# Kernel tuning notes

Measured on AMD Instinct MI355X. Metric: run time of the kernel, lower is better.

## Reference

```python
import jax, jax.numpy as jnp
import numpy as np

D_MODEL = 1024
N_HEADS = 16
D_KEYS = 64
D_LLM = 4096
B, L, S = 8, 1024, 1000
HD = N_HEADS * D_KEYS  # 1024


def setup_inputs() -> dict:
    key = jax.random.key(0)
    ks = jax.random.split(key, 12)
    sd = lambda fan_in: 1.0 / np.sqrt(fan_in)
    return {
        "target_embedding": jax.random.normal(ks[0], (B, L, D_MODEL), jnp.float32),
        "source_embedding": jax.random.normal(ks[1], (S, D_LLM), jnp.float32),
        "value_embedding": jax.random.normal(ks[2], (S, D_LLM), jnp.float32),
        "Wq": jax.random.normal(ks[3], (D_MODEL, HD), jnp.float32) * sd(D_MODEL),
        "bq": jnp.zeros((HD,), jnp.float32),
        "Wk": jax.random.normal(ks[4], (D_LLM, HD), jnp.float32) * sd(D_LLM),
        "bk": jnp.zeros((HD,), jnp.float32),
        "Wv": jax.random.normal(ks[5], (D_LLM, HD), jnp.float32) * sd(D_LLM),
        "bv": jnp.zeros((HD,), jnp.float32),
        "Wo": jax.random.normal(ks[6], (HD, D_LLM), jnp.float32) * sd(HD),
        "bo": jnp.zeros((D_LLM,), jnp.float32),
        "alpha": jnp.asarray(1.0, jnp.float32),
        "beta": jnp.asarray(0.5, jnp.float32),
    }


def reference(target_embedding, source_embedding, value_embedding,
              Wq, bq, Wk, bk, Wv, bv, Wo, bo, alpha, beta):
    # Projections
    q = (target_embedding @ Wq + bq).reshape(B, L, N_HEADS, D_KEYS)   # blhe
    k = (source_embedding @ Wk + bk).reshape(S, N_HEADS, D_KEYS)      # she
    v = (value_embedding @ Wv + bv).reshape(S, N_HEADS, D_KEYS)       # she
    # Reprogramming attention with alpha/beta scaling
    scale = 1.0 / np.sqrt(D_KEYS)
    scores = jnp.einsum('blhe,she->bhls', alpha * q, beta * k)        # BxHxLxS
    A = jax.nn.softmax(scale * scores, axis=-1)  # dropout is identity in eval
    out = jnp.einsum('bhls,she->blhe', A, v)
    out = out.reshape(B, L, HD)
    return out @ Wo + bo                                              # B,L,d_llm
```

## Files before the change

kernel.cpp:

```cpp
#include <hip/hip_runtime.h>

typedef unsigned short u16;
typedef __attribute__((ext_vector_type(8))) short short8;
typedef __attribute__((ext_vector_type(4))) float floatx4;

#define LOG2E 1.4426950408889634f

__device__ __forceinline__ u16 f2bf(float f) {
    unsigned u = __builtin_bit_cast(unsigned, f);
    u += 0x7fffu + ((u >> 16) & 1u);
    return (u16)(u >> 16);
}

__device__ __forceinline__ void gl2lds16(const void* g, void* l) {
    __builtin_amdgcn_global_load_lds((const __attribute__((address_space(1))) void*)g,
                                     (__attribute__((address_space(3))) void*)l,
                                     16, 0, 0);
}

__global__ __launch_bounds__(256) void conv_all(const float* __restrict__ T, u16* __restrict__ Tb,
                                                const float* __restrict__ Se, u16* __restrict__ Seb,
                                                const float* __restrict__ Ve, u16* __restrict__ Veb) {
    int g = blockIdx.x * 256 + threadIdx.x;
    const float* s; u16* d; int i; int nsrc;
    if (g < 2097152)      { s = T;  d = Tb;  i = g * 4;               nsrc = 8388608; }
    else if (g < 3145728) { s = Se; d = Seb; i = (g - 2097152) * 4;   nsrc = 4096000; }
    else                  { s = Ve; d = Veb; i = (g - 3145728) * 4;   nsrc = 4096000; }
    ushort4 o;
    if (i < nsrc) {
        float4 v = *(const float4*)(s + i);
        o.x = f2bf(v.x); o.y = f2bf(v.y); o.z = f2bf(v.z); o.w = f2bf(v.w);
    } else {
        o = make_ushort4(0, 0, 0, 0);
    }
    *(ushort4*)(d + i) = o;
}

__device__ __forceinline__ void transpose_core(const float* __restrict__ W, u16* __restrict__ Wt,
                                               int Kd, int Nd, int kx, int ny) {
    __shared__ u16 t[64][65];
    const int tid = threadIdx.x;
    const int k0 = kx * 64, n0 = ny * 64;
#pragma unroll
    for (int i = 0; i < 16; i++) {
        int r = i * 4 + (tid >> 6), c = tid & 63;
        t[r][c] = f2bf(W[(size_t)(k0 + r) * Nd + n0 + c]);
    }
    __syncthreads();
#pragma unroll
    for (int i = 0; i < 16; i++) {
        int n = i * 4 + (tid >> 6), k = tid & 63;
        Wt[(size_t)(n0 + n) * Kd + k0 + k] = t[k][n];
    }
}

__global__ __launch_bounds__(256) void transpose3(const float* __restrict__ Wq, u16* __restrict__ WqT,
                                                  const float* __restrict__ Wk, u16* __restrict__ WkT,
                                                  const float* __restrict__ Wv, u16* __restrict__ WvT) {
    int id = blockIdx.x;
    if (id < 256)       transpose_core(Wq, WqT, 1024, 1024, id & 15, id >> 4);
    else if (id < 1280) { int t = id - 256;  transpose_core(Wk, WkT, 4096, 1024, t & 63, t >> 6); }
    else                { int t = id - 1280; transpose_core(Wv, WvT, 4096, 1024, t & 63, t >> 6); }
}


__device__ __forceinline__ short8 ldsfrag(const u16* b, int row, int kk, int quad, int l7) {
    return *(const short8*)&b[row * 64 + (((kk * 4 + quad) ^ l7) * 8)];
}

__device__ __forceinline__
void stage_tile(u16* dA, u16* dB, const u16* gA, const u16* gB, int Ks, int wave, int lane) {
    int rl = wave * 8 + (lane >> 3);
    int cs = ((lane & 7) ^ (rl & 7)) * 8;
#pragma unroll
    for (int ii = 0; ii < 4; ii++) {
        gl2lds16(gA + (size_t)(ii * 64 + rl) * Ks + cs, dA + ii * 4096 + wave * 512);
        gl2lds16(gB + (size_t)(ii * 64 + rl) * Ks + cs, dB + ii * 4096 + wave * 512);
    }
}

__device__ __forceinline__
void four_phases(const u16* sA, const u16* sB, floatx4 (&acc)[8][4],
                 int wm, int wn, int quad, int l16, int l7,
                 bool stage, u16* dA, u16* dB, const u16* gA, const u16* gB, int Ks,
                 int wave, int lane) {
    short8 af[4][2], b0[2][2], b1[2][2];
    const int ra = wm * 128 + l16, rb = wn * 64 + l16;

#pragma unroll
    for (int i = 0; i < 4; i++) {
        af[i][0] = ldsfrag(sA, ra + i * 16, 0, quad, l7);
        af[i][1] = ldsfrag(sA, ra + i * 16, 1, quad, l7);
    }
#pragma unroll
    for (int j = 0; j < 2; j++) {
        b0[j][0] = ldsfrag(sB, rb + j * 16, 0, quad, l7);
        b0[j][1] = ldsfrag(sB, rb + j * 16, 1, quad, l7);
    }
    if (stage) stage_tile(dA, dB, gA, gB, Ks, wave, lane);
    __builtin_amdgcn_s_barrier();
    __builtin_amdgcn_s_setprio(1);
#pragma unroll
    for (int k = 0; k < 2; k++)
#pragma unroll
        for (int i = 0; i < 4; i++)
#pragma unroll
            for (int j = 0; j < 2; j++)
                acc[i][j] = __builtin_amdgcn_mfma_f32_16x16x32_bf16(af[i][k], b0[j][k], acc[i][j], 0, 0, 0);
    __builtin_amdgcn_s_setprio(0);
    __builtin_amdgcn_s_barrier();

#pragma unroll
    for (int j = 0; j < 2; j++) {
        b1[j][0] = ldsfrag(sB, rb + (j + 2) * 16, 0, quad, l7);
        b1[j][1] = ldsfrag(sB, rb + (j + 2) * 16, 1, quad, l7);
    }
    __builtin_amdgcn_s_barrier();
    __builtin_amdgcn_s_setprio(1);
#pragma unroll
    for (int k = 0; k < 2; k++)
#pragma unroll
        for (int i = 0; i < 4; i++)
#pragma unroll
            for (int j = 0; j < 2; j++)
                acc[i][j + 2] = __builtin_amdgcn_mfma_f32_16x16x32_bf16(af[i][k], b1[j][k], acc[i][j + 2], 0, 0, 0);
    __builtin_amdgcn_s_setprio(0);
    __builtin_amdgcn_s_barrier();

#pragma unroll
    for (int i = 0; i < 4; i++) {
        af[i][0] = ldsfrag(sA, ra + (i + 4) * 16, 0, quad, l7);
        af[i][1] = ldsfrag(sA, ra + (i + 4) * 16, 1, quad, l7);
    }
    __builtin_amdgcn_s_barrier();
    __builtin_amdgcn_s_setprio(1);
#pragma unroll
    for (int k = 0; k < 2; k++)
#pragma unroll
        for (int i = 0; i < 4; i++)
#pragma unroll
            for (int j = 0; j < 2; j++)
                acc[i + 4][j + 2] = __builtin_amdgcn_mfma_f32_16x16x32_bf16(af[i][k], b1[j][k], acc[i + 4][j + 2], 0, 0, 0);
    __builtin_amdgcn_s_setprio(0);
    __builtin_amdgcn_s_barrier();

    __builtin_amdgcn_s_setprio(1);
#pragma unroll
    for (int k = 0; k < 2; k++)
#pragma unroll
        for (int i = 0; i < 4; i++)
#pragma unroll
            for (int j = 0; j < 2; j++)
                acc[i + 4][j] = __builtin_amdgcn_mfma_f32_16x16x32_bf16(af[i][k], b0[j][k], acc[i + 4][j], 0, 0, 0);
    __builtin_amdgcn_s_setprio(0);
}

__device__ __forceinline__
void gemm8_core(const u16* __restrict__ A, const u16* __restrict__ Bt,
                const float* __restrict__ bias, void* __restrict__ Cout,
                int M, int N, int Ks, int Klen, int koff,
                int mode, float mult, int m0, int n0, u16* lds) {
    const int tid = threadIdx.x;
    const int wave = tid >> 6, lane = tid & 63;
    const int quad = lane >> 4, l16 = lane & 15, l7 = l16 & 7;
    const int wm = wave >> 2, wn = wave & 3;

    u16* A0 = lds;          u16* B0 = lds + 16384;
    u16* A1 = lds + 32768;  u16* B1 = lds + 49152;

    floatx4 acc[8][4];
#pragma unroll
    for (int i = 0; i < 8; i++)
#pragma unroll
        for (int j = 0; j < 4; j++) acc[i][j] = (floatx4){0.f, 0.f, 0.f, 0.f};

    const u16* Ag = A + (size_t)m0 * Ks + koff;
    const u16* Bg = Bt + (size_t)n0 * Ks + koff;

    stage_tile(A0, B0, Ag, Bg, Ks, wave, lane);
    asm volatile("s_waitcnt vmcnt(0)" ::: "memory");
    __builtin_amdgcn_sched_barrier(0);
    __builtin_amdgcn_s_barrier();

    const int NIT = Klen >> 7;
#pragma unroll 1
    for (int it = 0; it < NIT; ++it) {
        four_phases(A0, B0, acc, wm, wn, quad, l16, l7,
                    true, A1, B1, Ag + (2 * it + 1) * 64, Bg + (2 * it + 1) * 64, Ks, wave, lane);
        asm volatile("s_waitcnt vmcnt(0)" ::: "memory");
        __builtin_amdgcn_sched_barrier(0);
        __builtin_amdgcn_s_barrier();
        four_phases(A1, B1, acc, wm, wn, quad, l16, l7,
                    it + 1 < NIT, A0, B0, Ag + (2 * it + 2) * 64, Bg + (2 * it + 2) * 64, Ks, wave, lane);
        asm volatile("s_waitcnt vmcnt(0)" ::: "memory");
        __builtin_amdgcn_sched_barrier(0);
        __builtin_amdgcn_s_barrier();
    }

#pragma unroll
    for (int i = 0; i < 8; i++) {
#pragma unroll
        for (int j = 0; j < 4; j++) {
            int col = n0 + wn * 64 + j * 16 + l16;
            float bvv = (mode >= 4) ? 0.0f : bias[col];
#pragma unroll
            for (int r = 0; r < 4; r++) {
                int row = m0 + wm * 128 + i * 16 + quad * 4 + r;
                float v = (acc[i][j][r] + bvv) * mult;
                if (mode == 3 || mode == 4) {
                    ((float*)Cout)[(size_t)row * N + col] = v;
                } else if (mode == 5) {
                    ((float*)Cout)[(size_t)col * M + row] = v;
                } else {
                    ((u16*)Cout)[(size_t)row * N + col] = f2bf(v);
                }
            }
        }
    }
}

__global__ __launch_bounds__(512, 2)
void gemm_qkv(const u16* __restrict__ Tb, const u16* __restrict__ WqT, const float* __restrict__ bq,
              const u16* __restrict__ Seb, const u16* __restrict__ WkT,
              const u16* __restrict__ Veb, const u16* __restrict__ WvT,
              u16* __restrict__ Qb, float* __restrict__ KP, float* __restrict__ VPT,
              const float* __restrict__ alphaP, const float* __restrict__ betaP) {
    __shared__ u16 lds[65536];
    int b0 = blockIdx.x;
    int w = (b0 & 7) * 32 + (b0 >> 3);
    if (w < 128) {
        float mult = alphaP[0] * betaP[0] * 0.125f * LOG2E;
        gemm8_core(Tb, WqT, bq, Qb, 8192, 1024, 1024, 1024, 0,
                   1, mult, (w >> 2) * 256, (w & 3) * 256, lds);
    } else if (w < 192) {
        int t = w - 128; int kc = t >> 4;
        gemm8_core(Seb, WkT, nullptr, KP + (size_t)kc * 1048576, 1024, 1024, 4096, 1024, kc * 1024,
                   4, 1.0f, ((t >> 2) & 3) * 256, (t & 3) * 256, lds);
    } else {
        int t = w - 192; int kc = t >> 4;
        gemm8_core(Veb, WvT, nullptr, VPT + (size_t)kc * 1048576, 1024, 1024, 4096, 1024, kc * 1024,
                   5, 1.0f, ((t >> 2) & 3) * 256, (t & 3) * 256, lds);
    }
}

__global__ __launch_bounds__(512, 2)
void gemm_final(const u16* __restrict__ A, const u16* __restrict__ Bt,
                const float* __restrict__ bias, float* __restrict__ Cout) {
    __shared__ u16 lds[65536];
    int b0 = blockIdx.x;
    int idx = b0 >> 3;
    int m = (b0 & 7) * 4 + (idx >> 4);
    int n = idx & 15;
    gemm8_core(A, Bt, bias, Cout, 8192, 4096, 1024, 1024, 0, 3, 1.0f, m * 256, n * 256, lds);
}

__global__ __launch_bounds__(256)
void reduce_wo(const float* __restrict__ KP, const float* __restrict__ bk, u16* __restrict__ Kb,
               const float* __restrict__ VPT, const float* __restrict__ bv, u16* __restrict__ VTb,
               const float* __restrict__ Wo, u16* __restrict__ WoT) {
    int id = blockIdx.x;
    if (id >= 2048) {
        int t = id - 2048;
        transpose_core(Wo, WoT, 1024, 4096, t & 15, t >> 4);
        return;
    }
    const int tid = threadIdx.x;
    if (id < 1024) {
        int r = id, c = tid * 4;
        size_t base = (size_t)r * 1024 + c;
        float4 a0 = *(const float4*)(KP + base);
        float4 a1 = *(const float4*)(KP + 1048576 + base);
        float4 a2 = *(const float4*)(KP + 2097152 + base);
        float4 a3 = *(const float4*)(KP + 3145728 + base);
        float4 bb = *(const float4*)(bk + c);
        ushort4 o;
        o.x = f2bf(a0.x + a1.x + a2.x + a3.x + bb.x);
        o.y = f2bf(a0.y + a1.y + a2.y + a3.y + bb.y);
        o.z = f2bf(a0.z + a1.z + a2.z + a3.z + bb.z);
        o.w = f2bf(a0.w + a1.w + a2.w + a3.w + bb.w);
        *(ushort4*)(Kb + base) = o;
    } else {
        int d = id - 1024, s = tid * 4;
        size_t base = (size_t)d * 1024 + s;
        float4 a0 = *(const float4*)(VPT + base);
        float4 a1 = *(const float4*)(VPT + 1048576 + base);
        float4 a2 = *(const float4*)(VPT + 2097152 + base);
        float4 a3 = *(const float4*)(VPT + 3145728 + base);
        float bvv = bv[d];
        ushort4 o;
        o.x = f2bf(a0.x + a1.x + a2.x + a3.x + bvv);
        o.y = f2bf(a0.y + a1.y + a2.y + a3.y + bvv);
        o.z = f2bf(a0.z + a1.z + a2.z + a3.z + bvv);
        o.w = f2bf(a0.w + a1.w + a2.w + a3.w + bvv);
        *(ushort4*)(VTb + base) = o;
    }
}

__global__ __launch_bounds__(256, 2)
void attn_kernel(const u16* __restrict__ Q, const u16* __restrict__ Kb,
                 const u16* __restrict__ VT, u16* __restrict__ O) {
    __shared__ u16 sK[128 * 64];
    __shared__ u16 sV[64 * 128];
    __shared__ u16 sP[128 * 128];
    const int tid = threadIdx.x;
    const int wave = tid >> 6, lane = tid & 63;
    const int quad = lane >> 4, l16 = lane & 15;
    const int l7 = l16 & 7;
    const int bid = blockIdx.x;
    const int qt = bid & 7, h = (bid >> 3) & 15, b = bid >> 7;

    const u16* Qbase = Q + ((size_t)(b * 1024 + qt * 128 + wave * 32)) * 1024 + h * 64;
    short8 qf[2][2];
#pragma unroll
    for (int i = 0; i < 2; i++)
#pragma unroll
        for (int kk = 0; kk < 2; kk++)
            qf[i][kk] = *(const short8*)&Qbase[(size_t)(i * 16 + l16) * 1024 + kk * 32 + quad * 8];

    float psum[2] = {0.f, 0.f};
    floatx4 oacc[2][4];
#pragma unroll
    for (int i = 0; i < 2; i++)
#pragma unroll
        for (int n = 0; n < 4; n++) oacc[i][n] = (floatx4){0.f, 0.f, 0.f, 0.f};

    for (int st = 0; st < 8; ++st) {
#pragma unroll
        for (int i = 0; i < 4; i++) {
            int r = i * 32 + wave * 8 + (lane >> 3);
            int c = ((lane & 7) ^ ((lane >> 3) & 7)) * 8;
            gl2lds16(Kb + (size_t)(st * 128 + r) * 1024 + h * 64 + c, sK + i * 2048 + wave * 512);
        }
#pragma unroll
        for (int i = 0; i < 4; i++) {
            int r = i * 16 + wave * 4 + (lane >> 4);
            int c = ((lane & 15) ^ ((wave * 4 + (lane >> 4)) & 7)) * 8;
            gl2lds16(VT + (size_t)(h * 64 + r) * 1024 + st * 128 + c, sV + i * 2048 + wave * 512);
        }
        __syncthreads();

        floatx4 sacc[2][8];
#pragma unroll
        for (int i = 0; i < 2; i++)
#pragma unroll
            for (int j = 0; j < 8; j++) sacc[i][j] = (floatx4){0.f, 0.f, 0.f, 0.f};
#pragma unroll
        for (int kk = 0; kk < 2; kk++) {
            short8 kf[8];
#pragma unroll
            for (int j = 0; j < 8; j++)
                kf[j] = *(const short8*)&sK[(j * 16 + l16) * 64 + (((kk * 4 + quad) ^ l7) * 8)];
#pragma unroll
            for (int i = 0; i < 2; i++)
#pragma unroll
                for (int j = 0; j < 8; j++)
                    sacc[i][j] = __builtin_amdgcn_mfma_f32_16x16x32_bf16(kf[j], qf[i][kk], sacc[i][j], 0, 0, 0);
        }

#pragma unroll
        for (int i = 0; i < 2; i++) {
            const int rowbase = (wave * 32 + i * 16 + l16) * 128;
#pragma unroll
            for (int j = 0; j < 8; j++) {
                float p0 = exp2f(sacc[i][j][0]);
                float p1 = exp2f(sacc[i][j][1]);
                float p2 = exp2f(sacc[i][j][2]);
                float p3 = exp2f(sacc[i][j][3]);
                if (st == 7) {
                    if (j == 7 || (j == 6 && quad >= 2)) { p0 = p1 = p2 = p3 = 0.f; }
                }
                psum[i] += (p0 + p1) + (p2 + p3);
                uint2 val;
                val.x = (unsigned)f2bf(p0) | ((unsigned)f2bf(p1) << 16);
                val.y = (unsigned)f2bf(p2) | ((unsigned)f2bf(p3) << 16);
                int chunk = (2 * j + (quad >> 1)) ^ l7;
                *(uint2*)&sP[rowbase + chunk * 8 + (quad & 1) * 4] = val;
            }
        }

#pragma unroll
        for (int c = 0; c < 4; c++) {
            short8 pf[2], vf[4];
#pragma unroll
            for (int i = 0; i < 2; i++)
                pf[i] = *(const short8*)&sP[(wave * 32 + i * 16 + l16) * 128 + (((c * 4 + quad) ^ l7) * 8)];
#pragma unroll
            for (int n = 0; n < 4; n++)
                vf[n] = *(const short8*)&sV[(n * 16 + l16) * 128 + (((c * 4 + quad) ^ l7) * 8)];
#pragma unroll
            for (int i = 0; i < 2; i++)
#pragma unroll
                for (int n = 0; n < 4; n++)
                    oacc[i][n] = __builtin_amdgcn_mfma_f32_16x16x32_bf16(pf[i], vf[n], oacc[i][n], 0, 0, 0);
        }
        __syncthreads();
    }

#pragma unroll
    for (int i = 0; i < 2; i++) {
        psum[i] += __shfl_xor(psum[i], 16);
        psum[i] += __shfl_xor(psum[i], 32);
    }

    u16* Obase = O + ((size_t)(b * 1024 + qt * 128 + wave * 32)) * 1024 + h * 64;
#pragma unroll
    for (int i = 0; i < 2; i++) {
#pragma unroll
        for (int r = 0; r < 4; r++) {
            float l = __shfl(psum[i], (lane & 48) | (quad * 4 + r));
            float linv = 1.0f / l;
#pragma unroll
            for (int n = 0; n < 4; n++)
                Obase[(size_t)(i * 16 + quad * 4 + r) * 1024 + n * 16 + l16] = f2bf(oacc[i][n][r] * linv);
        }
    }
}

extern "C" void kernel_launch(void* const* d_in, const int* in_sizes, int n_in,
                              void* d_out, int out_size, void* d_ws, size_t ws_size,
                              hipStream_t stream) {
    const float* T     = (const float*)d_in[0];
    const float* Se    = (const float*)d_in[1];
    const float* Ve    = (const float*)d_in[2];
    const float* Wq    = (const float*)d_in[3];
    const float* bq    = (const float*)d_in[4];
    const float* Wk    = (const float*)d_in[5];
    const float* bk    = (const float*)d_in[6];
    const float* Wv    = (const float*)d_in[7];
    const float* bv    = (const float*)d_in[8];
    const float* Wo    = (const float*)d_in[9];
    const float* bo    = (const float*)d_in[10];
    const float* alpha = (const float*)d_in[11];
    const float* beta  = (const float*)d_in[12];

    char* ws = (char*)d_ws;
    size_t off = 0;
    auto alloc = [&](size_t bytes) { size_t o = off; off += (bytes + 255) & ~(size_t)255; return o; };

    u16* Tb  = (u16*)(ws + alloc((size_t)8192 * 1024 * 2));
    u16* Seb = (u16*)(ws + alloc((size_t)1024 * 4096 * 2));
    u16* Veb = (u16*)(ws + alloc((size_t)1024 * 4096 * 2));
    u16* WqT = (u16*)(ws + alloc((size_t)1024 * 1024 * 2));
    u16* WkT = (u16*)(ws + alloc((size_t)1024 * 4096 * 2));
    u16* WvT = (u16*)(ws + alloc((size_t)1024 * 4096 * 2));
    u16* Qb  = (u16*)(ws + alloc((size_t)8192 * 1024 * 2));
    u16* Kb  = (u16*)(ws + alloc((size_t)1024 * 1024 * 2));
    u16* VTb = (u16*)(ws + alloc((size_t)1024 * 1024 * 2));
    float* KP  = (float*)(ws + alloc((size_t)4 * 1024 * 1024 * 4));
    float* VPT = (float*)(ws + alloc((size_t)4 * 1024 * 1024 * 4));
    u16* Ob  = Tb;
    u16* WoT = Veb;

    conv_all<<<16384, 256, 0, stream>>>(T, Tb, Se, Seb, Ve, Veb);
    transpose3<<<2304, 256, 0, stream>>>(Wq, WqT, Wk, WkT, Wv, WvT);
    gemm_qkv<<<256, 512, 0, stream>>>(Tb, WqT, bq, Seb, WkT, Veb, WvT,
                                      Qb, KP, VPT, alpha, beta);
    reduce_wo<<<3072, 256, 0, stream>>>(KP, bk, Kb, VPT, bv, VTb, Wo, WoT);
    attn_kernel<<<1024, 256, 0, stream>>>(Qb, Kb, VTb, Ob);
    gemm_final<<<512, 512, 0, stream>>>(Ob, WoT, bo, (float*)d_out);
}
```

Measured before the change: 458.6 us.

## Restructure GEMM mainloop into K-halves with finer-grained async staging

Replaces the four-phase, 128-wide K iteration with a 64-wide K tile split into two 32-wide halves, each staged separately into LDS via direct global-to-LDS loads. Partial vmcnt waits overlap loading the next halves with MFMA work on the current ones. LDS fragments are now read from an unswizzled 32-column layout, dropping the XOR swizzle. This trades fewer barriers and shorter waits for possible LDS bank conflicts, and it is correct only if the vmcnt counting matches the outstanding loads.

New measurement: 433.1 us. 5.6% less time.

```diff
diff --git a/kernel.cpp b/kernel.cpp
--- a/kernel.cpp
+++ b/kernel.cpp
@@ -64,95 +64,18 @@
 }
 
 
-__device__ __forceinline__ short8 ldsfrag(const u16* b, int row, int kk, int quad, int l7) {
-    return *(const short8*)&b[row * 64 + (((kk * 4 + quad) ^ l7) * 8)];
-}
-
 __device__ __forceinline__
-void stage_tile(u16* dA, u16* dB, const u16* gA, const u16* gB, int Ks, int wave, int lane) {
-    int rl = wave * 8 + (lane >> 3);
-    int cs = ((lane & 7) ^ (rl & 7)) * 8;
-#pragma unroll
-    for (int ii = 0; ii < 4; ii++) {
-        gl2lds16(gA + (size_t)(ii * 64 + rl) * Ks + cs, dA + ii * 4096 + wave * 512);
-        gl2lds16(gB + (size_t)(ii * 64 + rl) * Ks + cs, dB + ii * 4096 + wave * 512);
-    }
-}
-
-__device__ __forceinline__
-void four_phases(const u16* sA, const u16* sB, floatx4 (&acc)[8][4],
-                 int wm, int wn, int quad, int l16, int l7,
-                 bool stage, u16* dA, u16* dB, const u16* gA, const u16* gB, int Ks,
-                 int wave, int lane) {
-    short8 af[4][2], b0[2][2], b1[2][2];
-    const int ra = wm * 128 + l16, rb = wn * 64 + l16;
-
-#pragma unroll
-    for (int i = 0; i < 4; i++) {
-        af[i][0] = ldsfrag(sA, ra + i * 16, 0, quad, l7);
-        af[i][1] = ldsfrag(sA, ra + i * 16, 1, quad, l7);
-    }
-#pragma unroll
-    for (int j = 0; j < 2; j++) {
-        b0[j][0] = ldsfrag(sB, rb + j * 16, 0, quad, l7);
-        b0[j][1] = ldsfrag(sB, rb + j * 16, 1, quad, l7);
-    }
-    if (stage) stage_tile(dA, dB, gA, gB, Ks, wave, lane);
-    __builtin_amdgcn_s_barrier();
-    __builtin_amdgcn_s_setprio(1);
-#pragma unroll
-    for (int k = 0; k < 2; k++)
-#pragma unroll
-        for (int i = 0; i < 4; i++)
-#pragma unroll
-            for (int j = 0; j < 2; j++)
-                acc[i][j] = __builtin_amdgcn_mfma_f32_16x16x32_bf16(af[i][k], b0[j][k], acc[i][j], 0, 0, 0);
-    __builtin_amdgcn_s_setprio(0);
-    __builtin_amdgcn_s_barrier();
-
-#pragma unroll
-    for (int j = 0; j < 2; j++) {
-        b1[j][0] = ldsfrag(sB, rb + (j + 2) * 16, 0, quad, l7);
-        b1[j][1] = ldsfrag(sB, rb + (j + 2) * 16, 1, quad, l7);
-    }
-    __builtin_amdgcn_s_barrier();
-    __builtin_amdgcn_s_setprio(1);
-#pragma unroll
-    for (int k = 0; k < 2; k++)
-#pragma unroll
-        for (int i = 0; i < 4; i++)
-#pragma unroll
-            for (int j = 0; j < 2; j++)
-                acc[i][j + 2] = __builtin_amdgcn_mfma_f32_16x16x32_bf16(af[i][k], b1[j][k], acc[i][j + 2], 0, 0, 0);
-    __builtin_amdgcn_s_setprio(0);
-    __builtin_amdgcn_s_barrier();
-
-#pragma unroll
-    for (int i = 0; i < 4; i++) {
-        af[i][0] = ldsfrag(sA, ra + (i + 4) * 16, 0, quad, l7);
-        af[i][1] = ldsfrag(sA, ra + (i + 4) * 16, 1, quad, l7);
-    }
-    __builtin_amdgcn_s_barrier();
-    __builtin_amdgcn_s_setprio(1);
-#pragma unroll
-    for (int k = 0; k < 2; k++)
-#pragma unroll
-        for (int i = 0; i < 4; i++)
-#pragma unroll
-            for (int j = 0; j < 2; j++)
-                acc[i + 4][j + 2] = __builtin_amdgcn_mfma_f32_16x16x32_bf16(af[i][k], b1[j][k], acc[i + 4][j + 2], 0, 0, 0);
-    __builtin_amdgcn_s_setprio(0);
-    __builtin_amdgcn_s_barrier();
-
-    __builtin_amdgcn_s_setprio(1);
-#pragma unroll
-    for (int k = 0; k < 2; k++)
-#pragma unroll
-        for (int i = 0; i < 4; i++)
-#pragma unroll
-            for (int j = 0; j < 2; j++)
-                acc[i + 4][j] = __builtin_amdgcn_mfma_f32_16x16x32_bf16(af[i][k], b0[j][k], acc[i + 4][j], 0, 0, 0);
-    __builtin_amdgcn_s_setprio(0);
+void stage_half(u16* dstA, u16* dstB, const u16* gA, const u16* gB, int Ks, int wave, int lane) {
+    int r = lane >> 2;
+    int cp = (lane & 3) * 8;
+    const u16* a0 = gA + (size_t)(wave * 32 + r) * Ks + cp;
+    const u16* b0 = gB + (size_t)(wave * 32 + r) * Ks + cp;
+    const u16* a1 = gA + (size_t)(wave * 32 + 16 + r) * Ks + cp;
+    const u16* b1 = gB + (size_t)(wave * 32 + 16 + r) * Ks + cp;
+    gl2lds16(a0, dstA + wave * 1024);
+    gl2lds16(b0, dstB + wave * 1024);
+    gl2lds16(a1, dstA + wave * 1024 + 512);
+    gl2lds16(b1, dstB + wave * 1024 + 512);
 }
 
 __device__ __forceinline__
@@ -162,11 +85,8 @@
                 int mode, float mult, int m0, int n0, u16* lds) {
     const int tid = threadIdx.x;
     const int wave = tid >> 6, lane = tid & 63;
-    const int quad = lane >> 4, l16 = lane & 15, l7 = l16 & 7;
+    const int quad = lane >> 4, l16 = lane & 15;
     const int wm = wave >> 2, wn = wave & 3;
-
-    u16* A0 = lds;          u16* B0 = lds + 16384;
-    u16* A1 = lds + 32768;  u16* B1 = lds + 49152;
 
     floatx4 acc[8][4];
 #pragma unroll
@@ -176,25 +96,77 @@
 
     const u16* Ag = A + (size_t)m0 * Ks + koff;
     const u16* Bg = Bt + (size_t)n0 * Ks + koff;
-
-    stage_tile(A0, B0, Ag, Bg, Ks, wave, lane);
-    asm volatile("s_waitcnt vmcnt(0)" ::: "memory");
-    __builtin_amdgcn_sched_barrier(0);
-    __builtin_amdgcn_s_barrier();
-
-    const int NIT = Klen >> 7;
+    const int NT = Klen >> 6;
+
+    const int raw = (wm * 128 + l16) * 32 + quad * 8;
+    const int rbw = (wn * 64 + l16) * 32 + quad * 8;
+
+    stage_half(lds, lds + 16384, Ag, Bg, Ks, wave, lane);
+    stage_half(lds + 8192, lds + 24576, Ag + 32, Bg + 32, Ks, wave, lane);
+
 #pragma unroll 1
-    for (int it = 0; it < NIT; ++it) {
-        four_phases(A0, B0, acc, wm, wn, quad, l16, l7,
-                    true, A1, B1, Ag + (2 * it + 1) * 64, Bg + (2 * it + 1) * 64, Ks, wave, lane);
-        asm volatile("s_waitcnt vmcnt(0)" ::: "memory");
+    for (int t = 0; t < NT; ++t) {
+        u16* cur = lds + (t & 1) * 32768;
+        u16* nxt = lds + ((t + 1) & 1) * 32768;
+        const u16* An = Ag + (size_t)(t + 1) * 64;
+        const u16* Bn = Bg + (size_t)(t + 1) * 64;
+        const bool st = (t + 1 < NT);
+        short8 af[4], bf[4];
+
+        asm volatile("s_waitcnt vmcnt(4)" ::: "memory");
         __builtin_amdgcn_sched_barrier(0);
         __builtin_amdgcn_s_barrier();
-        four_phases(A1, B1, acc, wm, wn, quad, l16, l7,
-                    it + 1 < NIT, A0, B0, Ag + (2 * it + 2) * 64, Bg + (2 * it + 2) * 64, Ks, wave, lane);
-        asm volatile("s_waitcnt vmcnt(0)" ::: "memory");
+#pragma unroll
+        for (int i = 0; i < 4; i++) af[i] = *(const short8*)&cur[raw + i * 512];
+#pragma unroll
+        for (int j = 0; j < 4; j++) bf[j] = *(const short8*)&cur[16384 + rbw + j * 512];
+        if (st) stage_half(nxt, nxt + 16384, An, Bn, Ks, wave, lane);
+        __builtin_amdgcn_s_setprio(1);
+#pragma unroll
+        for (int i = 0; i < 4; i++)
+#pragma unroll
+            for (int j = 0; j < 4; j++)
+                acc[i][j] = __builtin_amdgcn_mfma_f32_16x16x32_bf16(af[i], bf[j], acc[i][j], 0, 0, 0);
+        __builtin_amdgcn_s_setprio(0);
+
+        __builtin_amdgcn_s_barrier();
+#pragma unroll
+        for (int i = 0; i < 4; i++) af[i] = *(const short8*)&cur[raw + 2048 + i * 512];
+        __builtin_amdgcn_s_setprio(1);
+#pragma unroll
+        for (int i = 0; i < 4; i++)
+#pragma unroll
+            for (int j = 0; j < 4; j++)
+                acc[i + 4][j] = __builtin_amdgcn_mfma_f32_16x16x32_bf16(af[i], bf[j], acc[i + 4][j], 0, 0, 0);
+        __builtin_amdgcn_s_setprio(0);
+
+        if (st) { asm volatile("s_waitcnt vmcnt(4)" ::: "memory"); }
+        else    { asm volatile("s_waitcnt vmcnt(0)" ::: "memory"); }
         __builtin_amdgcn_sched_barrier(0);
         __builtin_amdgcn_s_barrier();
+#pragma unroll
+        for (int i = 0; i < 4; i++) af[i] = *(const short8*)&cur[8192 + raw + i * 512];
+#pragma unroll
+        for (int j = 0; j < 4; j++) bf[j] = *(const short8*)&cur[24576 + rbw + j * 512];
+        if (st) stage_half(nxt + 8192, nxt + 24576, An + 32, Bn + 32, Ks, wave, lane);
+        __builtin_amdgcn_s_setprio(1);
+#pragma unroll
+        for (int i = 0; i < 4; i++)
+#pragma unroll
+            for (int j = 0; j < 4; j++)
+                acc[i][j] = __builtin_amdgcn_mfma_f32_16x16x32_bf16(af[i], bf[j], acc[i][j], 0, 0, 0);
+        __builtin_amdgcn_s_setprio(0);
+
+        __builtin_amdgcn_s_barrier();
+#pragma unroll
+        for (int i = 0; i < 4; i++) af[i] = *(const short8*)&cur[8192 + raw + 2048 + i * 512];
+        __builtin_amdgcn_s_setprio(1);
+#pragma unroll
+        for (int i = 0; i < 4; i++)
+#pragma unroll
+            for (int j = 0; j < 4; j++)
+                acc[i + 4][j] = __builtin_amdgcn_mfma_f32_16x16x32_bf16(af[i], bf[j], acc[i + 4][j], 0, 0, 0);
+        __builtin_amdgcn_s_setprio(0);
     }
 
 #pragma unroll
```
